# Optimization experiments

Hardware: AMD Instinct MI355X
Metric: run time of the kernel (lower is better)

## Reference

```python
import jax, jax.numpy as jnp
import numpy as np

B, V, N, S, F, H, K, STEPS = 8, 3, 400, 1200, 16, 32, 10, 12
ALPHA_FUSE = 0.8
NEG = -9e15


def setup_inputs() -> dict:
    key = jax.random.key(0)
    ks = jax.random.split(key, 16)
    g = lambda i, shape, s=0.1: jax.random.normal(ks[i], shape, jnp.float32) * s
    return {
        "feat": jax.random.normal(ks[0], (B, S, F), jnp.float32),
        "adj": jax.random.bernoulli(ks[1], 0.05, (B, V, S, S)).astype(jnp.float32),
        "dis_lab": jax.random.uniform(ks[2], (B, K), dtype=jnp.float32),
        "W_gat": g(3, (V, F, H), 0.3),
        "a_gat": g(4, (V, 2 * H, 1), 0.3),
        "qkv_W": g(5, (H, 3 * H)),
        "qkv_b": jnp.zeros((3 * H,), jnp.float32),
        "o_W": g(6, (H, H)),
        "o_b": jnp.zeros((H,), jnp.float32),
        "fus_W": g(7, (H, H)),
        "fus_b": jnp.zeros((H,), jnp.float32),
        "att1_W": g(8, (2 * H, H)),
        "att1_b": jnp.zeros((H,), jnp.float32),
        "att2_W": g(9, (H, 1)),
        "att2_b": jnp.zeros((1,), jnp.float32),
        "gru_Wih": g(10, (H, 3 * H)),
        "gru_Whh": g(11, (H, 3 * H)),
        "gru_bih": jnp.zeros((3 * H,), jnp.float32),
        "gru_bhh": jnp.zeros((3 * H,), jnp.float32),
        "out_W": g(12, (H, 1)),
        "out_b": jnp.zeros((1,), jnp.float32),
    }


def _forward(feat, adj, dis_lab, W_gat, a_gat, qkv_W, qkv_b, o_W, o_b,
             fus_W, fus_b, att1_W, att1_b, att2_W, att2_b,
             gru_Wih, gru_Whh, gru_bih, gru_bhh, out_W, out_b):
    # ---- per-view GAT (masked softmax over dense adjacency) ----
    Wh = jnp.einsum('bsf,vfh->bvsh', feat, W_gat)            # [B,V,S,H]
    a1, a2 = a_gat[:, :H, 0], a_gat[:, H:, 0]
    e = (jnp.einsum('bvsh,vh->bvs', Wh, a1)[..., :, None]
         + jnp.einsum('bvsh,vh->bvs', Wh, a2)[..., None, :])  # [B,V,S,S]
    e = jax.nn.leaky_relu(e, 0.2)
    e = jnp.where(adj > 0, e, NEG)
    att = jax.nn.softmax(e, axis=-1)
    hid = jax.nn.elu(jnp.einsum('bvst,bvth->bvsh', att, Wh))  # [B,V,S,H]
    # ---- cross-view self-attention fusion (single head) ----
    x = hid.reshape(B, V * S, H)
    q, k, v = jnp.split(x @ qkv_W + qkv_b, 3, axis=-1)
    logits = jnp.einsum('bld,bmd->blm', q, k) / jnp.sqrt(jnp.float32(H))
    sa = jnp.einsum('blm,bmd->bld', jax.nn.softmax(logits, axis=-1), v)
    sa = sa @ o_W + o_b
    hfuse = (ALPHA_FUSE * sa + (1.0 - ALPHA_FUSE) * x).reshape(B, V, S, H)
    gate = jax.nn.sigmoid(hfuse @ fus_W + fus_b)
    fusion = jnp.sum(gate * hfuse, axis=1)[:, 2 * N:, :]      # [B,N,H]
    # ---- attention over label stations ----
    label = fusion[:, :K, :]                                  # [B,K,H]
    unlabel = fusion[:, K, :]                                 # [B,H]
    cat = jnp.concatenate([label, jnp.broadcast_to(unlabel[:, None, :], label.shape)], axis=-1)
    s = jax.nn.relu(cat @ att1_W + att1_b) @ att2_W + att2_b  # [B,K,1]
    score = jax.nn.softmax(s[..., 0] * dis_lab, axis=1)
    ctx = jnp.einsum('bk,bkh->bh', score, label)
    # ---- GRU decoder (feed hidden state back as next input) ----
    def gru_cell(xt, h):
        gi = xt @ gru_Wih + gru_bih
        gh = h @ gru_Whh + gru_bhh
        ir, iz, inn = jnp.split(gi, 3, axis=-1)
        hr, hz, hn = jnp.split(gh, 3, axis=-1)
        r = jax.nn.sigmoid(ir + hr)
        z = jax.nn.sigmoid(iz + hz)
        n = jnp.tanh(inn + r * hn)
        return (1.0 - z) * n + z * h
    def step(carry, _):
        xt, h = carry
        h2 = gru_cell(xt, h)
        out = h2 @ out_W + out_b
        return (h2, h2), out[:, 0]
    _, outs = jax.lax.scan(step, (ctx, unlabel), None, length=STEPS)
    return outs.T  # [B, STEPS]


def reference(feat, adj, dis_lab, W_gat, a_gat, qkv_W, qkv_b, o_W, o_b,
              fus_W, fus_b, att1_W, att1_b, att2_W, att2_b,
              gru_Wih, gru_Whh, gru_bih, gru_bhh, out_W, out_b):
    return _forward(feat, adj, dis_lab, W_gat, a_gat, qkv_W, qkv_b, o_W, o_b,
                    fus_W, fus_b, att1_W, att1_b, att2_W, att2_b,
                    gru_Wih, gru_Whh, gru_bih, gru_bhh, out_W, out_b)
```

## Files before the change

### kernel.cpp

```cpp
#include <hip/hip_runtime.h>
#include <math.h>

#define Bb 8
#define Vv 3
#define Ss 1200
#define Ff 16
#define Hh 32
#define Kk 10
#define STEPS 12
#define ROWS (Bb*Vv*Ss)
#define L (Vv*Ss)
#define KPAD 1216
#define MW 38

typedef __attribute__((ext_vector_type(8))) short bf16x8;
typedef __attribute__((ext_vector_type(4))) float f32x4;
typedef __attribute__((ext_vector_type(4))) unsigned int u32x4;

__device__ __forceinline__ unsigned int pack_hi2(float x0, float x1) {
    return (__float_as_uint(x1) & 0xFFFF0000u) | (__float_as_uint(x0) >> 16);
}
__device__ __forceinline__ unsigned int pack_lo2(float x0, float x1) {
    float h0 = __uint_as_float(__float_as_uint(x0) & 0xFFFF0000u);
    float h1 = __uint_as_float(__float_as_uint(x1) & 0xFFFF0000u);
    return (__float_as_uint(x1 - h1) & 0xFFFF0000u) | (__float_as_uint(x0 - h0) >> 16);
}

__global__ __launch_bounds__(256) void gat_wh_k(const float* __restrict__ feat,
                                                const float* __restrict__ W_gat,
                                                const float* __restrict__ a_gat,
                                                float* __restrict__ Wh,
                                                float* __restrict__ fvec,
                                                float* __restrict__ gvec) {
    int blk = blockIdx.x;
    int c = blk % 150;
    int v = (blk / 150) % Vv;
    int b = blk / (150 * Vv);
    int tid = threadIdx.x;
    int r = tid >> 5;
    int h = tid & 31;
    int s = c * 8 + r;

    __shared__ float Wg[16][32];
    __shared__ float fe[8][16];
    for (int i = tid; i < 512; i += 256) Wg[i >> 5][i & 31] = W_gat[v * 512 + i];
    for (int i = tid; i < 128; i += 256) fe[i >> 4][i & 15] = feat[(b * Ss + c * 8) * Ff + i];
    __syncthreads();

    float acc = 0.f;
#pragma unroll
    for (int k = 0; k < 16; ++k) acc += fe[r][k] * Wg[k][h];

    int row = (b * Vv + v) * Ss + s;
    Wh[(size_t)row * Hh + h] = acc;

    float a1 = a_gat[v * 64 + h];
    float a2 = a_gat[v * 64 + 32 + h];
    float pf = acc * a1, pg = acc * a2;
#pragma unroll
    for (int m = 16; m >= 1; m >>= 1) {
        pf += __shfl_xor(pf, m);
        pg += __shfl_xor(pg, m);
    }
    if (h == 0) { fvec[row] = pf; gvec[row] = pg; }
}

__global__ __launch_bounds__(256) void gmax_k(const float* __restrict__ gvec,
                                              float* __restrict__ Gmax) {
    int bv = blockIdx.x;
    int tid = threadIdx.x;
    float m = -3.0e38f;
    for (int t = tid; t < Ss; t += 256) m = fmaxf(m, gvec[bv * Ss + t]);
#pragma unroll
    for (int mm = 32; mm >= 1; mm >>= 1) m = fmaxf(m, __shfl_xor(m, mm));
    __shared__ float red[4];
    if ((tid & 63) == 0) red[tid >> 6] = m;
    __syncthreads();
    if (tid == 0) Gmax[bv] = fmaxf(fmaxf(red[0], red[1]), fmaxf(red[2], red[3]));
}

__global__ __launch_bounds__(256) void wht_k(const float* __restrict__ Wh,
                                             ushort* __restrict__ WhT_hi,
                                             ushort* __restrict__ WhT_lo) {
    int bv = blockIdx.x / 19, t = blockIdx.x % 19;
    int s0 = t * 64;
    int tid = threadIdx.x;
    __shared__ float T[64][33];
    for (int idx = tid; idx < 2048; idx += 256) {
        int r = idx >> 5, h = idx & 31;
        T[r][h] = (s0 + r < Ss) ? Wh[((size_t)bv * Ss + s0 + r) * Hh + h] : 0.f;
    }
    __syncthreads();
    int h = tid >> 3, c = tid & 7;
    unsigned int hb[4], lb[4];
#pragma unroll
    for (int j = 0; j < 4; ++j) {
        float e0 = T[c * 8 + 2 * j][h], e1 = T[c * 8 + 2 * j + 1][h];
        hb[j] = pack_hi2(e0, e1);
        lb[j] = pack_lo2(e0, e1);
    }
    size_t off = ((size_t)bv * 32 + h) * KPAD + s0 + c * 8;
    *(uint4*)(WhT_hi + off) = make_uint4(hb[0], hb[1], hb[2], hb[3]);
    *(uint4*)(WhT_lo + off) = make_uint4(lb[0], lb[1], lb[2], lb[3]);
}

__global__ __launch_bounds__(320) void adj_pack_k(const float* __restrict__ adj,
                                                  unsigned int* __restrict__ maskb) {
    int row = blockIdx.x;
    int tid = threadIdx.x;
    __shared__ unsigned char nib[320];
    unsigned char n = 0;
    if (tid < 300) {
        float4 a = ((const float4*)(adj + (size_t)row * Ss))[tid];
        n = (a.x > 0.f ? 1u : 0u) | (a.y > 0.f ? 2u : 0u) |
            (a.z > 0.f ? 4u : 0u) | (a.w > 0.f ? 8u : 0u);
    }
    nib[tid] = n;
    __syncthreads();
    if (tid < MW) {
        unsigned int m = 0;
#pragma unroll
        for (int i = 0; i < 8; ++i) m |= ((unsigned int)nib[tid * 8 + i]) << (4 * i);
        maskb[(size_t)row * MW + tid] = m;
    }
}

__global__ __launch_bounds__(256) void gat_mfma_k(const unsigned int* __restrict__ maskb,
                                                  const ushort* __restrict__ WhT_hi,
                                                  const ushort* __restrict__ WhT_lo,
                                                  const float* __restrict__ fvec,
                                                  const float* __restrict__ gvec,
                                                  const float* __restrict__ Gmax,
                                                  float* __restrict__ hid,
                                                  float* __restrict__ hsel) {
    int blk = blockIdx.x;
    int bv = blk / 75, tb = blk % 75;
    int wk = threadIdx.x >> 6, lane = threadIdx.x & 63;
    int rowbase = tb * 16;
    int lr = lane & 15, kg = lane >> 4;
    int b = bv / Vv, v = bv - b * Vv;

    int ar = rowbase + lr;
    const float* g_b = gvec + (size_t)bv * Ss;
    const unsigned int* mrow = maskb + (size_t)(bv * Ss + ar) * MW;
    float fr = fvec[bv * Ss + ar];
    float M = fr + Gmax[bv];
    float Mr = fmaxf(M, 0.2f * M);

    f32x4 acc0 = {0.f, 0.f, 0.f, 0.f}, acc1 = {0.f, 0.f, 0.f, 0.f};
    float psum = 0.f;
    const ushort* Bh0 = WhT_hi + ((size_t)bv * 32 + lr) * KPAD;
    const ushort* Bl0 = WhT_lo + ((size_t)bv * 32 + lr) * KPAD;

    int kst = wk * 320;
    int kend = kst + 320; if (kend > KPAD) kend = KPAD;
    for (int k0 = kst; k0 < kend; k0 += 32) {
        int t0 = k0 + kg * 8;
        bf16x8 bh0 = *(const bf16x8*)(Bh0 + t0);
        bf16x8 bl0 = *(const bf16x8*)(Bl0 + t0);
        bf16x8 bh1 = *(const bf16x8*)(Bh0 + 16 * KPAD + t0);
        bf16x8 bl1 = *(const bf16x8*)(Bl0 + 16 * KPAD + t0);

        unsigned int mbyte = (mrow[k0 >> 5] >> (kg * 8)) & 0xFFu;
        float gv8[8];
        if (t0 + 8 <= Ss) {
            float4 gA = *(const float4*)(g_b + t0);
            float4 gB = *(const float4*)(g_b + t0 + 4);
            gv8[0] = gA.x; gv8[1] = gA.y; gv8[2] = gA.z; gv8[3] = gA.w;
            gv8[4] = gB.x; gv8[5] = gB.y; gv8[6] = gB.z; gv8[7] = gB.w;
        } else {
#pragma unroll
            for (int j = 0; j < 8; ++j) gv8[j] = (t0 + j < Ss) ? g_b[t0 + j] : 0.f;
        }
        float p[8];
#pragma unroll
        for (int j = 0; j < 8; ++j) {
            float e = fr + gv8[j];
            e = fmaxf(e, 0.2f * e);
            float pe = __expf(e - Mr);
            p[j] = ((mbyte >> j) & 1u) ? pe : 0.f;
            psum += p[j];
        }
        unsigned int hb[4], lb[4];
#pragma unroll
        for (int j = 0; j < 4; ++j) {
            hb[j] = pack_hi2(p[2 * j], p[2 * j + 1]);
            lb[j] = pack_lo2(p[2 * j], p[2 * j + 1]);
        }
        bf16x8 ah = __builtin_bit_cast(bf16x8, (u32x4){hb[0], hb[1], hb[2], hb[3]});
        bf16x8 al = __builtin_bit_cast(bf16x8, (u32x4){lb[0], lb[1], lb[2], lb[3]});
        acc0 = __builtin_amdgcn_mfma_f32_16x16x32_bf16(ah, bh0, acc0, 0, 0, 0);
        acc0 = __builtin_amdgcn_mfma_f32_16x16x32_bf16(ah, bl0, acc0, 0, 0, 0);
        acc0 = __builtin_amdgcn_mfma_f32_16x16x32_bf16(al, bh0, acc0, 0, 0, 0);
        acc1 = __builtin_amdgcn_mfma_f32_16x16x32_bf16(ah, bh1, acc1, 0, 0, 0);
        acc1 = __builtin_amdgcn_mfma_f32_16x16x32_bf16(ah, bl1, acc1, 0, 0, 0);
        acc1 = __builtin_amdgcn_mfma_f32_16x16x32_bf16(al, bh1, acc1, 0, 0, 0);
    }

    psum += __shfl_xor(psum, 16);
    psum += __shfl_xor(psum, 32);

    __shared__ float accS[4][2][16][17];
    __shared__ float psS[4][16];
#pragma unroll
    for (int j = 0; j < 4; ++j) {
        accS[wk][0][kg * 4 + j][lr] = acc0[j];
        accS[wk][1][kg * 4 + j][lr] = acc1[j];
    }
    if (lane < 16) psS[wk][lr] = psum;
    __syncthreads();
    if (threadIdx.x < 16)
        psS[0][threadIdx.x] += psS[1][threadIdx.x] + psS[2][threadIdx.x] + psS[3][threadIdx.x];
    __syncthreads();

    bool qb = (tb == 50);
    for (int idx = threadIdx.x; idx < 512; idx += 256) {
        int r = idx >> 5, col = idx & 31, tt = col >> 4, c = col & 15;
        float a = accS[0][tt][r][c] + accS[1][tt][r][c] + accS[2][tt][r][c] + accS[3][tt][r][c];
        float rr = a / psS[0][r];
        float hv = (rr > 0.f) ? rr : expm1f(rr);
        hid[((size_t)bv * Ss + rowbase + r) * 32 + col] = hv;
        if (qb && r < 11) hsel[(((size_t)b * Vv + v) * 11 + r) * 32 + col] = hv;
    }
}

#define CH 120
#define NCH 30
#define PREC 34
__global__ __launch_bounds__(256) void attn_part_k(const float* __restrict__ hid,
                                                   const float* __restrict__ hsel,
                                                   const float* __restrict__ qkv_W,
                                                   const float* __restrict__ qkv_b,
                                                   float* __restrict__ part) {
    int blk = blockIdx.x;
    int b = blk / NCH, ch = blk % NCH;
    int k0 = ch * CH;
    int tid = threadIdx.x;
    const float inv = 0.1767766952966369f;

    __shared__ float hC[CH][33];
    __shared__ float hq[33][33];
    __shared__ float W1[32][33];
    __shared__ float W2[32][33];
    __shared__ float qS[33][33];
    __shared__ float qt[33][33];
    __shared__ float qc[33];
    __shared__ float lS[33][124];
    __shared__ float mS[33], lsS[33];

    for (int idx = tid; idx < CH * 32; idx += 256) {
        int r = idx >> 5, i = idx & 31;
        hC[r][i] = hid[((size_t)b * L + k0 + r) * 32 + i];
    }
    for (int idx = tid; idx < 33 * 32; idx += 256) {
        int q = idx >> 5, i = idx & 31;
        int si = q / 3, v = q - si * 3;
        hq[q][i] = hsel[(((size_t)b * Vv + v) * 11 + si) * 32 + i];
    }
    for (int idx = tid; idx < 1024; idx += 256) {
        int i = idx >> 5, j = idx & 31;
        W1[i][j] = qkv_W[i * 96 + j];
        W2[i][j] = qkv_W[i * 96 + 32 + j];
    }
    __syncthreads();
    for (int idx = tid; idx < 33 * 32; idx += 256) {
        int q = idx >> 5, j = idx & 31;
        float a = qkv_b[j];
#pragma unroll
        for (int i = 0; i < 32; ++i) a += hq[q][i] * W1[i][j];
        qS[q][j] = a;
    }
    __syncthreads();
    for (int idx = tid; idx < 33 * 32; idx += 256) {
        int q = idx >> 5, i = idx & 31;
        float a = 0.f;
#pragma unroll
        for (int j = 0; j < 32; ++j) a += qS[q][j] * W2[i][j];
        qt[q][i] = a;
    }
    if (tid < 33) {
        float a = 0.f;
        for (int j = 0; j < 32; ++j) a += qS[tid][j] * qkv_b[32 + j];
        qc[tid] = a;
    }
    __syncthreads();

    for (int idx = tid; idx < 33 * CH; idx += 256) {
        int q = idx / CH, m = idx - q * CH;
        float d = 0.f;
#pragma unroll
        for (int i = 0; i < 32; ++i) d += qt[q][i] * hC[m][i];
        lS[q][m] = (d + qc[q]) * inv;
    }
    __syncthreads();

    int q4 = tid >> 2, j4 = tid & 3;
    if (q4 < 33) {
        float m = -3.0e38f;
        for (int k = j4; k < CH; k += 4) m = fmaxf(m, lS[q4][k]);
        m = fmaxf(m, __shfl_xor(m, 1));
        m = fmaxf(m, __shfl_xor(m, 2));
        float ssum = 0.f;
        for (int k = j4; k < CH; k += 4) {
            float p = __expf(lS[q4][k] - m);
            lS[q4][k] = p;
            ssum += p;
        }
        ssum += __shfl_xor(ssum, 1);
        ssum += __shfl_xor(ssum, 2);
        if (j4 == 0) { mS[q4] = m; lsS[q4] = ssum; }
    }
    __syncthreads();

    float* po = part + ((size_t)b * NCH + ch) * (33 * PREC);
    for (int idx = tid; idx < 33 * 32; idx += 256) {
        int q = idx >> 5, hh = idx & 31;
        float a = 0.f;
        for (int k = 0; k < CH; k += 4) {
            float4 p4 = *(const float4*)&lS[q][k];
            a += p4.x * hC[k][hh] + p4.y * hC[k+1][hh] + p4.z * hC[k+2][hh] + p4.w * hC[k+3][hh];
        }
        po[q * PREC + hh] = a;
    }
    if (tid < 33) { po[tid * PREC + 32] = mS[tid]; po[tid * PREC + 33] = lsS[tid]; }
}

__global__ __launch_bounds__(256) void attn_comb_k(const float* __restrict__ part,
                                                   const float* __restrict__ hsel,
                                                   const float* __restrict__ qkv_W,
                                                   const float* __restrict__ qkv_b,
                                                   const float* __restrict__ o_W,
                                                   const float* __restrict__ o_b,
                                                   const float* __restrict__ fus_W,
                                                   const float* __restrict__ fus_b,
                                                   float* __restrict__ hfg) {
    int b = blockIdx.x;
    int tid = threadIdx.x;
    __shared__ float RS[33][NCH];
    __shared__ float LSs[33];
    __shared__ float oS[33][33];
    __shared__ float vS[33][33];
    __shared__ float hfS[33][33];
    const float* pb = part + (size_t)b * NCH * (33 * PREC);

    if (tid < 33) {
        float M = -3.0e38f;
        for (int c = 0; c < NCH; ++c) M = fmaxf(M, pb[c * 33 * PREC + tid * PREC + 32]);
        float Lt = 0.f;
        for (int c = 0; c < NCH; ++c) {
            float w = __expf(pb[c * 33 * PREC + tid * PREC + 32] - M);
            RS[tid][c] = w;
            Lt += w * pb[c * 33 * PREC + tid * PREC + 33];
        }
        LSs[tid] = Lt;
    }
    __syncthreads();

    for (int idx = tid; idx < 33 * 32; idx += 256) {
        int q = idx >> 5, hh = idx & 31;
        float a = 0.f;
        for (int c = 0; c < NCH; ++c) a += RS[q][c] * pb[c * 33 * PREC + q * PREC + hh];
        oS[q][hh] = a / LSs[q];
    }
    __syncthreads();
    for (int idx = tid; idx < 33 * 32; idx += 256) {
        int q = idx >> 5, j = idx & 31;
        float a = qkv_b[64 + j];
#pragma unroll
        for (int i = 0; i < 32; ++i) a += oS[q][i] * qkv_W[i * 96 + 64 + j];
        vS[q][j] = a;
    }
    __syncthreads();
    for (int idx = tid; idx < 33 * 32; idx += 256) {
        int q = idx >> 5, hh = idx & 31;
        int si = q / 3, v = q - si * 3;
        float o = o_b[hh];
#pragma unroll
        for (int i = 0; i < 32; ++i) o += vS[q][i] * o_W[i * 32 + hh];
        float x = hsel[(((size_t)b * Vv + v) * 11 + si) * Hh + hh];
        hfS[q][hh] = 0.8f * o + 0.2f * x;
    }
    __syncthreads();
    for (int idx = tid; idx < 33 * 32; idx += 256) {
        int q = idx >> 5, hh = idx & 31;
        float gacc = fus_b[hh];
#pragma unroll
        for (int i = 0; i < 32; ++i) gacc += hfS[q][i] * fus_W[i * 32 + hh];
        float gate = 1.f / (1.f + __expf(-gacc));
        hfg[(size_t)(b * 33 + q) * 32 + hh] = gate * hfS[q][hh];
    }
}

__global__ __launch_bounds__(64) void head_k(const float* __restrict__ hfg,
                                             const float* __restrict__ dis_lab,
                                             const float* __restrict__ att1_W,
                                             const float* __restrict__ att1_b,
                                             const float* __restrict__ att2_W,
                                             const float* __restrict__ att2_b,
                                             const float* __restrict__ Wih,
                                             const float* __restrict__ Whh,
                                             const float* __restrict__ bih,
                                             const float* __restrict__ bhh,
                                             const float* __restrict__ out_W,
                                             const float* __restrict__ out_b,
                                             float* __restrict__ out) {
    int b = blockIdx.x;
    int tid = threadIdx.x;
    int j = tid & 31, half = tid >> 5;

    __shared__ float lab[11][32];
    __shared__ float a1T[32][68];
    __shared__ float WihT[3][32][36];
    __shared__ float WhhT[3][32][36];
    __shared__ float sc[12];
    __shared__ float xS[32], hS[32];

    for (int i = tid; i < 352; i += 64) {
        int k = i >> 5, hh = i & 31;
        float val = 0.f;
#pragma unroll
        for (int v = 0; v < 3; ++v) val += hfg[(size_t)(b * 33 + k * 3 + v) * 32 + hh];
        lab[k][hh] = val;
    }
    for (int idx = tid; idx < 2048; idx += 64) {
        int i = idx >> 5, jj = idx & 31;
        a1T[jj][i] = att1_W[idx];
    }
    for (int idx = tid; idx < 3072; idx += 64) {
        int i = idx / 96, col = idx - i * 96;
        int g = col >> 5, jj = col & 31;
        WihT[g][jj][i] = Wih[idx];
        WhhT[g][jj][i] = Whh[idx];
    }
    __syncthreads();

    float a2w = att2_W[j];
    float a1b = att1_b[j];
    float a2b = att2_b[0];
#pragma unroll
    for (int kk = 0; kk < 5; ++kk) {
        int k = 2 * kk + half;
        float t1 = a1b;
#pragma unroll
        for (int c = 0; c < 8; ++c) {
            float4 lb4 = *(const float4*)&lab[k][c * 4];
            float4 w4  = *(const float4*)&a1T[j][c * 4];
            t1 += lb4.x * w4.x + lb4.y * w4.y + lb4.z * w4.z + lb4.w * w4.w;
        }
#pragma unroll
        for (int c = 0; c < 8; ++c) {
            float4 lb4 = *(const float4*)&lab[10][c * 4];
            float4 w4  = *(const float4*)&a1T[j][32 + c * 4];
            t1 += lb4.x * w4.x + lb4.y * w4.y + lb4.z * w4.z + lb4.w * w4.w;
        }
        float val = fmaxf(t1, 0.f) * a2w;
#pragma unroll
        for (int mm = 16; mm >= 1; mm >>= 1) val += __shfl_xor(val, mm);
        if (j == 0) sc[k] = (val + a2b) * dis_lab[b * Kk + k];
    }
    __syncthreads();
    if (tid == 0) {
        float mx = sc[0];
        for (int k = 1; k < 10; ++k) mx = fmaxf(mx, sc[k]);
        float sm = 0.f;
        for (int k = 0; k < 10; ++k) { sc[k] = __expf(sc[k] - mx); sm += sc[k]; }
        for (int k = 0; k < 10; ++k) sc[k] /= sm;
    }
    __syncthreads();
    if (tid < 32) {
        float c = 0.f;
        for (int k = 0; k < 10; ++k) c += sc[k] * lab[k][tid];
        xS[tid] = c;
        hS[tid] = lab[10][tid];
    }
    __syncthreads();

    float b_ir = bih[j], b_iz = bih[32 + j], b_in = bih[64 + j];
    float b_hr = bhh[j], b_hz = bhh[32 + j], b_hn = bhh[64 + j];
    float ow = out_W[j], ob = out_b[0];
    int i0 = half * 16;

    for (int t = 0; t < STEPS; ++t) {
        float gi_r = 0.f, gi_z = 0.f, gi_n = 0.f;
        float gh_r = 0.f, gh_z = 0.f, gh_n = 0.f;
#pragma unroll
        for (int c = 0; c < 4; ++c) {
            float4 x4 = *(const float4*)&xS[i0 + c * 4];
            float4 h4 = *(const float4*)&hS[i0 + c * 4];
            float4 wr = *(const float4*)&WihT[0][j][i0 + c * 4];
            float4 wz = *(const float4*)&WihT[1][j][i0 + c * 4];
            float4 wn = *(const float4*)&WihT[2][j][i0 + c * 4];
            float4 ur = *(const float4*)&WhhT[0][j][i0 + c * 4];
            float4 uz = *(const float4*)&WhhT[1][j][i0 + c * 4];
            float4 un = *(const float4*)&WhhT[2][j][i0 + c * 4];
            gi_r += x4.x * wr.x + x4.y * wr.y + x4.z * wr.z + x4.w * wr.w;
            gi_z += x4.x * wz.x + x4.y * wz.y + x4.z * wz.z + x4.w * wz.w;
            gi_n += x4.x * wn.x + x4.y * wn.y + x4.z * wn.z + x4.w * wn.w;
            gh_r += h4.x * ur.x + h4.y * ur.y + h4.z * ur.z + h4.w * ur.w;
            gh_z += h4.x * uz.x + h4.y * uz.y + h4.z * uz.z + h4.w * uz.w;
            gh_n += h4.x * un.x + h4.y * un.y + h4.z * un.z + h4.w * un.w;
        }
        gi_r += __shfl_xor(gi_r, 32); gi_z += __shfl_xor(gi_z, 32); gi_n += __shfl_xor(gi_n, 32);
        gh_r += __shfl_xor(gh_r, 32); gh_z += __shfl_xor(gh_z, 32); gh_n += __shfl_xor(gh_n, 32);

        float hprev = hS[j];
        float r = 1.f / (1.f + __expf(-(gi_r + b_ir + gh_r + b_hr)));
        float z = 1.f / (1.f + __expf(-(gi_z + b_iz + gh_z + b_hz)));
        float n = tanhf(gi_n + b_in + r * (gh_n + b_hn));
        float hnew = (1.f - z) * n + z * hprev;

        float outp = hnew * ow;
#pragma unroll
        for (int mm = 16; mm >= 1; mm >>= 1) outp += __shfl_xor(outp, mm);
        if (tid == 0) out[b * STEPS + t] = outp + ob;
        __syncthreads();
        if (tid < 32) { hS[tid] = hnew; xS[tid] = hnew; }
        __syncthreads();
    }
}

extern "C" void kernel_launch(void* const* d_in, const int* in_sizes, int n_in,
                              void* d_out, int out_size, void* d_ws, size_t ws_size,
                              hipStream_t stream) {
    const float* feat    = (const float*)d_in[0];
    const float* adj     = (const float*)d_in[1];
    const float* dis_lab = (const float*)d_in[2];
    const float* W_gat   = (const float*)d_in[3];
    const float* a_gat   = (const float*)d_in[4];
    const float* qkv_W   = (const float*)d_in[5];
    const float* qkv_b   = (const float*)d_in[6];
    const float* o_W     = (const float*)d_in[7];
    const float* o_b     = (const float*)d_in[8];
    const float* fus_W   = (const float*)d_in[9];
    const float* fus_b   = (const float*)d_in[10];
    const float* att1_W  = (const float*)d_in[11];
    const float* att1_b  = (const float*)d_in[12];
    const float* att2_W  = (const float*)d_in[13];
    const float* att2_b  = (const float*)d_in[14];
    const float* Wih     = (const float*)d_in[15];
    const float* Whh     = (const float*)d_in[16];
    const float* bih     = (const float*)d_in[17];
    const float* bhh     = (const float*)d_in[18];
    const float* out_W   = (const float*)d_in[19];
    const float* out_b   = (const float*)d_in[20];
    float* out = (float*)d_out;

    float* ws = (float*)d_ws;
    float*  Wh     = ws;
    float*  hid    = ws;
    float*  fvec   = ws + 921600;
    float*  gvec   = ws + 950400;
    float*  Gmax   = ws + 979200;
    ushort* WhT_hi = (ushort*)(ws + 979232);
    float*  part   = ws + 979232;
    ushort* WhT_lo = (ushort*)(ws + 1446176);
    float*  hsel   = ws + 1913120;
    float*  hfg    = ws + 1921568;
    unsigned int* maskb = (unsigned int*)(ws + 1930016);

    gat_wh_k<<<dim3(Bb * Vv * 150), dim3(256), 0, stream>>>(feat, W_gat, a_gat, Wh, fvec, gvec);
    gmax_k<<<dim3(Bb * Vv), dim3(256), 0, stream>>>(gvec, Gmax);
    wht_k<<<dim3(Bb * Vv * 19), dim3(256), 0, stream>>>(Wh, WhT_hi, WhT_lo);
    adj_pack_k<<<dim3(ROWS), dim3(320), 0, stream>>>(adj, maskb);
    gat_mfma_k<<<dim3(Bb * Vv * 75), dim3(256), 0, stream>>>(maskb, WhT_hi, WhT_lo,
                                                             fvec, gvec, Gmax, hid, hsel);
    attn_part_k<<<dim3(Bb * NCH), dim3(256), 0, stream>>>(hid, hsel, qkv_W, qkv_b, part);
    attn_comb_k<<<dim3(Bb), dim3(256), 0, stream>>>(part, hsel, qkv_W, qkv_b,
                                                    o_W, o_b, fus_W, fus_b, hfg);
    head_k<<<dim3(Bb), dim3(64), 0, stream>>>(hfg, dis_lab, att1_W, att1_b, att2_W, att2_b,
                                              Wih, Whh, bih, bhh, out_W, out_b, out);
}
```

Baseline: 149.9 us.

## Fuse adjacency mask into GAT MFMA kernel and hoist query projection

Drops the separate adjacency bit-packing kernel. The GAT MFMA kernel now reads the float adjacency rows directly and applies the mask inline, which removes one extra pass over the 138 MB adj tensor and one launch. It also moves the per-batch query projection (qt, qc) out of every attn_part block into a small dedicated kernel, so the 30 chunk blocks per batch no longer each redo it. In exchange the MFMA loop does wider uncoalesced-per-row float loads of adj, and there is one extra small launch.

```diff
diff --git a/kernel.cpp b/kernel.cpp
--- a/kernel.cpp
+++ b/kernel.cpp
@@ -11,7 +11,6 @@
 #define ROWS (Bb*Vv*Ss)
 #define L (Vv*Ss)
 #define KPAD 1216
-#define MW 38
 
 typedef __attribute__((ext_vector_type(8))) short bf16x8;
 typedef __attribute__((ext_vector_type(4))) float f32x4;
@@ -104,28 +103,7 @@
     *(uint4*)(WhT_lo + off) = make_uint4(lb[0], lb[1], lb[2], lb[3]);
 }
 
-__global__ __launch_bounds__(320) void adj_pack_k(const float* __restrict__ adj,
-                                                  unsigned int* __restrict__ maskb) {
-    int row = blockIdx.x;
-    int tid = threadIdx.x;
-    __shared__ unsigned char nib[320];
-    unsigned char n = 0;
-    if (tid < 300) {
-        float4 a = ((const float4*)(adj + (size_t)row * Ss))[tid];
-        n = (a.x > 0.f ? 1u : 0u) | (a.y > 0.f ? 2u : 0u) |
-            (a.z > 0.f ? 4u : 0u) | (a.w > 0.f ? 8u : 0u);
-    }
-    nib[tid] = n;
-    __syncthreads();
-    if (tid < MW) {
-        unsigned int m = 0;
-#pragma unroll
-        for (int i = 0; i < 8; ++i) m |= ((unsigned int)nib[tid * 8 + i]) << (4 * i);
-        maskb[(size_t)row * MW + tid] = m;
-    }
-}
-
-__global__ __launch_bounds__(256) void gat_mfma_k(const unsigned int* __restrict__ maskb,
+__global__ __launch_bounds__(256) void gat_mfma_k(const float* __restrict__ adj,
                                                   const ushort* __restrict__ WhT_hi,
                                                   const ushort* __restrict__ WhT_lo,
                                                   const float* __restrict__ fvec,
@@ -141,8 +119,8 @@
     int b = bv / Vv, v = bv - b * Vv;
 
     int ar = rowbase + lr;
+    const float* adj_r = adj + ((size_t)bv * Ss + ar) * Ss;
     const float* g_b = gvec + (size_t)bv * Ss;
-    const unsigned int* mrow = maskb + (size_t)(bv * Ss + ar) * MW;
     float fr = fvec[bv * Ss + ar];
     float M = fr + Gmax[bv];
     float Mr = fmaxf(M, 0.2f * M);
@@ -161,25 +139,25 @@
         bf16x8 bh1 = *(const bf16x8*)(Bh0 + 16 * KPAD + t0);
         bf16x8 bl1 = *(const bf16x8*)(Bl0 + 16 * KPAD + t0);
 
-        unsigned int mbyte = (mrow[k0 >> 5] >> (kg * 8)) & 0xFFu;
-        float gv8[8];
+        float p[8];
         if (t0 + 8 <= Ss) {
+            float4 aA = *(const float4*)(adj_r + t0);
+            float4 aB = *(const float4*)(adj_r + t0 + 4);
             float4 gA = *(const float4*)(g_b + t0);
             float4 gB = *(const float4*)(g_b + t0 + 4);
-            gv8[0] = gA.x; gv8[1] = gA.y; gv8[2] = gA.z; gv8[3] = gA.w;
-            gv8[4] = gB.x; gv8[5] = gB.y; gv8[6] = gB.z; gv8[7] = gB.w;
+            float av[8] = {aA.x, aA.y, aA.z, aA.w, aB.x, aB.y, aB.z, aB.w};
+            float gv[8] = {gA.x, gA.y, gA.z, gA.w, gB.x, gB.y, gB.z, gB.w};
+#pragma unroll
+            for (int j = 0; j < 8; ++j) {
+                float e = fr + gv[j];
+                e = fmaxf(e, 0.2f * e);
+                float pe = __expf(e - Mr);
+                p[j] = (av[j] > 0.f) ? pe : 0.f;
+                psum += p[j];
+            }
         } else {
 #pragma unroll
-            for (int j = 0; j < 8; ++j) gv8[j] = (t0 + j < Ss) ? g_b[t0 + j] : 0.f;
-        }
-        float p[8];
-#pragma unroll
-        for (int j = 0; j < 8; ++j) {
-            float e = fr + gv8[j];
-            e = fmaxf(e, 0.2f * e);
-            float pe = __expf(e - Mr);
-            p[j] = ((mbyte >> j) & 1u) ? pe : 0.f;
-            psum += p[j];
+            for (int j = 0; j < 8; ++j) p[j] = 0.f;
         }
         unsigned int hb[4], lb[4];
 #pragma unroll
@@ -224,13 +202,57 @@
     }
 }
 
+__global__ __launch_bounds__(256) void attn_q_k(const float* __restrict__ hsel,
+                                                const float* __restrict__ qkv_W,
+                                                const float* __restrict__ qkv_b,
+                                                float* __restrict__ qt,
+                                                float* __restrict__ qc) {
+    int b = blockIdx.x;
+    int tid = threadIdx.x;
+    __shared__ float hq[33][33];
+    __shared__ float W1[32][33];
+    __shared__ float W2[32][33];
+    __shared__ float qS[33][33];
+
+    for (int idx = tid; idx < 33 * 32; idx += 256) {
+        int q = idx >> 5, i = idx & 31;
+        int si = q / 3, v = q - si * 3;
+        hq[q][i] = hsel[(((size_t)b * Vv + v) * 11 + si) * 32 + i];
+    }
+    for (int idx = tid; idx < 1024; idx += 256) {
+        int i = idx >> 5, j = idx & 31;
+        W1[i][j] = qkv_W[i * 96 + j];
+        W2[i][j] = qkv_W[i * 96 + 32 + j];
+    }
+    __syncthreads();
+    for (int idx = tid; idx < 33 * 32; idx += 256) {
+        int q = idx >> 5, j = idx & 31;
+        float a = qkv_b[j];
+#pragma unroll
+        for (int i = 0; i < 32; ++i) a += hq[q][i] * W1[i][j];
+        qS[q][j] = a;
+    }
+    __syncthreads();
+    for (int idx = tid; idx < 33 * 32; idx += 256) {
+        int q = idx >> 5, i = idx & 31;
+        float a = 0.f;
+#pragma unroll
+        for (int j = 0; j < 32; ++j) a += qS[q][j] * W2[i][j];
+        qt[(size_t)b * 33 * 32 + q * 32 + i] = a;
+    }
+    if (tid < 33) {
+        float a = 0.f;
+        for (int j = 0; j < 32; ++j) a += qS[tid][j] * qkv_b[32 + j];
+        qc[b * 33 + tid] = a;
+    }
+}
+
 #define CH 120
 #define NCH 30
 #define PREC 34
 __global__ __launch_bounds__(256) void attn_part_k(const float* __restrict__ hid,
-                                                   const float* __restrict__ hsel,
-                                                   const float* __restrict__ qkv_W,
-                                                   const float* __restrict__ qkv_b,
+                                                   const float* __restrict__ qt,
+                                                   const float* __restrict__ qc,
                                                    float* __restrict__ part) {
     int blk = blockIdx.x;
     int b = blk / NCH, ch = blk % NCH;
@@ -239,12 +261,8 @@
     const float inv = 0.1767766952966369f;
 
     __shared__ float hC[CH][33];
-    __shared__ float hq[33][33];
-    __shared__ float W1[32][33];
-    __shared__ float W2[32][33];
-    __shared__ float qS[33][33];
-    __shared__ float qt[33][33];
-    __shared__ float qc[33];
+    __shared__ float qtS[33][33];
+    __shared__ float qcS[33];
     __shared__ float lS[33][124];
     __shared__ float mS[33], lsS[33];
 
@@ -254,43 +272,17 @@
     }
     for (int idx = tid; idx < 33 * 32; idx += 256) {
         int q = idx >> 5, i = idx & 31;
-        int si = q / 3, v = q - si * 3;
-        hq[q][i] = hsel[(((size_t)b * Vv + v) * 11 + si) * 32 + i];
-    }
-    for (int idx = tid; idx < 1024; idx += 256) {
-        int i = idx >> 5, j = idx & 31;
-        W1[i][j] = qkv_W[i * 96 + j];
-        W2[i][j] = qkv_W[i * 96 + 32 + j];
-    }
-    __syncthreads();
-    for (int idx = tid; idx < 33 * 32; idx += 256) {
-        int q = idx >> 5, j = idx & 31;
-        float a = qkv_b[j];
-#pragma unroll
-        for (int i = 0; i < 32; ++i) a += hq[q][i] * W1[i][j];
-        qS[q][j] = a;
-    }
-    __syncthreads();
-    for (int idx = tid; idx < 33 * 32; idx += 256) {
-        int q = idx >> 5, i = idx & 31;
-        float a = 0.f;
-#pragma unroll
-        for (int j = 0; j < 32; ++j) a += qS[q][j] * W2[i][j];
-        qt[q][i] = a;
-    }
-    if (tid < 33) {
-        float a = 0.f;
-        for (int j = 0; j < 32; ++j) a += qS[tid][j] * qkv_b[32 + j];
-        qc[tid] = a;
-    }
+        qtS[q][i] = qt[(size_t)b * 33 * 32 + q * 32 + i];
+    }
+    if (tid < 33) qcS[tid] = qc[b * 33 + tid];
     __syncthreads();
 
     for (int idx = tid; idx < 33 * CH; idx += 256) {
         int q = idx / CH, m = idx - q * CH;
         float d = 0.f;
 #pragma unroll
-        for (int i = 0; i < 32; ++i) d += qt[q][i] * hC[m][i];
-        lS[q][m] = (d + qc[q]) * inv;
+        for (int i = 0; i < 32; ++i) d += qtS[q][i] * hC[m][i];
+        lS[q][m] = (d + qcS[q]) * inv;
     }
     __syncthreads();
 
@@ -556,15 +548,16 @@
     ushort* WhT_lo = (ushort*)(ws + 1446176);
     float*  hsel   = ws + 1913120;
     float*  hfg    = ws + 1921568;
-    unsigned int* maskb = (unsigned int*)(ws + 1930016);
+    float*  qt     = ws + 1930016;
+    float*  qc     = ws + 1938464;
 
     gat_wh_k<<<dim3(Bb * Vv * 150), dim3(256), 0, stream>>>(feat, W_gat, a_gat, Wh, fvec, gvec);
     gmax_k<<<dim3(Bb * Vv), dim3(256), 0, stream>>>(gvec, Gmax);
     wht_k<<<dim3(Bb * Vv * 19), dim3(256), 0, stream>>>(Wh, WhT_hi, WhT_lo);
-    adj_pack_k<<<dim3(ROWS), dim3(320), 0, stream>>>(adj, maskb);
-    gat_mfma_k<<<dim3(Bb * Vv * 75), dim3(256), 0, stream>>>(maskb, WhT_hi, WhT_lo,
+    gat_mfma_k<<<dim3(Bb * Vv * 75), dim3(256), 0, stream>>>(adj, WhT_hi, WhT_lo,
                                                              fvec, gvec, Gmax, hid, hsel);
-    attn_part_k<<<dim3(Bb * NCH), dim3(256), 0, stream>>>(hid, hsel, qkv_W, qkv_b, part);
+    attn_q_k<<<dim3(Bb), dim3(256), 0, stream>>>(hsel, qkv_W, qkv_b, qt, qc);
+    attn_part_k<<<dim3(Bb * NCH), dim3(256), 0, stream>>>(hid, qt, qc, part);
     attn_comb_k<<<dim3(Bb), dim3(256), 0, stream>>>(part, hsel, qkv_W, qkv_b,
                                                     o_W, o_b, fus_W, fus_b, hfg);
     head_k<<<dim3(Bb), dim3(64), 0, stream>>>(hfg, dis_lab, att1_W, att1_b, att2_W, att2_b,
```

Result: faster. 139.0 us (-7.3%).
